# Performance work log

Hardware: AMD Instinct MI355X
Metric: run time of the kernel (lower is better)

## Reference

```python
import jax, jax.numpy as jnp
import numpy as np

B, D, LC, LQ = 16, 512, 2048, 512
NEG_INF = -1e30


def setup_inputs() -> dict:
    key = jax.random.key(0)
    k1, k2, k3 = jax.random.split(key, 3)
    C = jax.random.normal(k1, (B, D, LC), dtype=jnp.float32)
    Q = jax.random.normal(k2, (B, D, LQ), dtype=jnp.float32)
    cmask = jnp.ones((B, LC), dtype=bool)
    qmask = jnp.ones((B, LQ), dtype=bool)
    lim = np.sqrt(1.0 / D)
    w = jax.random.uniform(k3, (3 * D,), dtype=jnp.float32, minval=-lim, maxval=lim)
    return {"C": C, "Q": Q, "cmask": cmask, "qmask": qmask, "w": w}


def reference(C, Q, cmask, qmask, w):
    d = C.shape[1]
    Cb = jnp.swapaxes(C, 1, 2)  # (B, Lc, d)
    Qb = jnp.swapaxes(Q, 1, 2)  # (B, Lq, d)
    w1, w2, w3 = w[:d], w[d:2 * d], w[2 * d:]
    # Trilinear similarity, decomposed: S[b,i,j] = C_i.w1 + Q_j.w2 + (C_i*w3).Q_j
    S = (Cb @ w1)[:, :, None] + (Qb @ w2)[:, None, :] \
        + jnp.einsum('bid,bjd->bij', Cb * w3, Qb)  # (B, Lc, Lq)
    S1 = jax.nn.softmax(jnp.where(qmask[:, None, :], S, NEG_INF), axis=2)
    S2 = jax.nn.softmax(jnp.where(cmask[:, :, None], S, NEG_INF), axis=1)
    A = S1 @ Qb                                     # (B, Lc, d)
    Bt = (S1 @ jnp.swapaxes(S2, 1, 2)) @ Cb         # (B, Lc, d)
    out = jnp.concatenate([Cb, A, Cb * A, Cb * Bt], axis=2)  # (B, Lc, 4d)
    return jnp.swapaxes(out, 1, 2)  # (B, 4d, Lc); dropout inactive at inference
```

## Files before the change

kernel.cpp:

```cpp
#include <hip/hip_runtime.h>
#include <stdint.h>

#define Bn 16
#define Dn 512
#define LCn 2048
#define LQn 512

typedef __attribute__((ext_vector_type(8))) short s8v;
typedef __attribute__((ext_vector_type(4))) float f4v;

__device__ __forceinline__ unsigned short f2bf(float f) {
  union { float f; uint32_t u; } v; v.f = f;
  uint32_t r = v.u + 0x7FFFu + ((v.u >> 16) & 1u);
  return (unsigned short)(r >> 16);
}

__device__ __forceinline__ void async16(void* lds, const void* g) {
  __builtin_amdgcn_global_load_lds((const __attribute__((address_space(1))) void*)g,
                                   (__attribute__((address_space(3))) void*)lds, 16, 0, 0);
}

#define WAITVM(N) asm volatile("s_waitcnt vmcnt(" #N ")")
#define WAITLGKM(N) asm volatile("s_waitcnt lgkmcnt(" #N ")")
#define SCHEDBAR __builtin_amdgcn_sched_barrier(0)
#define BARRIER_LDS { WAITLGKM(0); SCHEDBAR; __builtin_amdgcn_s_barrier(); SCHEDBAR; }

typedef __attribute__((address_space(3))) const unsigned short* lds_csp;
__device__ __forceinline__ s8v ldsr(const unsigned short* p) {
  s8v r;
  asm volatile("ds_read_b128 %0, %1" : "=v"(r) : "v"((lds_csp)p));
  return r;
}



template <int KSTEPS>
__device__ __forceinline__ void gemm_core_p(const unsigned short* __restrict__ Ap,
                                            const unsigned short* __restrict__ Bp,
                                            unsigned short* As, unsigned short* Bs,
                                            f4v acc[4][4]) {
  const int t = threadIdx.x;
  const int lane = t & 63, quad = lane >> 4, l16 = lane & 15;
  const int wm = (t >> 6) & 1, wn = t >> 7;
  auto stage = [&](int buf, int ks) {
    const unsigned short* a = Ap + (size_t)ks * 4096;
    const unsigned short* b = Bp + (size_t)ks * 4096;
    async16(As + buf + t * 8, a + t * 8);
    async16(As + buf + (t + 256) * 8, a + 2048 + t * 8);
    async16(Bs + buf + t * 8, b + t * 8);
    async16(Bs + buf + (t + 256) * 8, b + 2048 + t * 8);
  };
  stage(0, 0);
  stage(4096, 1);
  for (int ks = 0; ks < KSTEPS; ++ks) {
    const int cur = (ks & 1) ? 4096 : 0;
    if (ks < KSTEPS - 1) { WAITVM(4); } else { WAITVM(0); }
    __builtin_amdgcn_s_barrier();
    SCHEDBAR;
    s8v af[4], bf[4];
#pragma unroll
    for (int mt = 0; mt < 4; ++mt)
      af[mt] = ldsr(As + cur + (wm * 64 + mt * 16 + l16) * 32 + quad * 8);
#pragma unroll
    for (int nt = 0; nt < 4; ++nt)
      bf[nt] = ldsr(Bs + cur + (wn * 64 + nt * 16 + l16) * 32 + quad * 8);
    WAITLGKM(0);
    SCHEDBAR;
    __builtin_amdgcn_s_barrier();
    SCHEDBAR;
    if (ks + 2 < KSTEPS) stage(cur, ks + 2);
    __builtin_amdgcn_s_setprio(1);
#pragma unroll
    for (int mt = 0; mt < 4; ++mt)
#pragma unroll
      for (int nt = 0; nt < 4; ++nt)
        acc[mt][nt] = __builtin_amdgcn_mfma_f32_16x16x32_bf16(af[mt], bf[nt], acc[mt][nt], 0, 0, 0);
    __builtin_amdgcn_s_setprio(0);
  }
}

template <int KSTEPS>
__device__ __forceinline__ void gemm_coreAB_p(const unsigned short* __restrict__ Ap,
                                              const unsigned short* __restrict__ Bp0,
                                              const unsigned short* __restrict__ Bp1,
                                              unsigned short* As, unsigned short* Bs0,
                                              unsigned short* Bs1,
                                              f4v accA[4][2], f4v accB[4][2]) {
  const int t = threadIdx.x;
  const int lane = t & 63, quad = lane >> 4, l16 = lane & 15;
  const int wm = (t >> 6) & 1, wn = t >> 7;
  auto stage = [&](int bufA, int bufB, int ks) {
    const unsigned short* a = Ap + (size_t)ks * 4096;
    async16(As + bufA + t * 8, a + t * 8);
    async16(As + bufA + (t + 256) * 8, a + 2048 + t * 8);
    async16(Bs0 + bufB + t * 8, Bp0 + (size_t)ks * 4096 + t * 8);
    async16(Bs1 + bufB + t * 8, Bp1 + (size_t)ks * 4096 + t * 8);
  };
  stage(0, 0, 0);
  stage(4096, 2048, 1);
  for (int ks = 0; ks < KSTEPS; ++ks) {
    const int curA = (ks & 1) ? 4096 : 0;
    const int curB = (ks & 1) ? 2048 : 0;
    if (ks < KSTEPS - 1) { WAITVM(4); } else { WAITVM(0); }
    __builtin_amdgcn_s_barrier();
    SCHEDBAR;
    s8v af[4], bq[2], bt[2];
#pragma unroll
    for (int mt = 0; mt < 4; ++mt)
      af[mt] = ldsr(As + curA + (wm * 64 + mt * 16 + l16) * 32 + quad * 8);
#pragma unroll
    for (int nt = 0; nt < 2; ++nt) {
      bq[nt] = ldsr(Bs0 + curB + (wn * 32 + nt * 16 + l16) * 32 + quad * 8);
      bt[nt] = ldsr(Bs1 + curB + (wn * 32 + nt * 16 + l16) * 32 + quad * 8);
    }
    WAITLGKM(0);
    SCHEDBAR;
    __builtin_amdgcn_s_barrier();
    SCHEDBAR;
    if (ks + 2 < KSTEPS) stage(curA, curB, ks + 2);
    __builtin_amdgcn_s_setprio(1);
#pragma unroll
    for (int mt = 0; mt < 4; ++mt)
#pragma unroll
      for (int nt = 0; nt < 2; ++nt) {
        accA[mt][nt] = __builtin_amdgcn_mfma_f32_16x16x32_bf16(af[mt], bq[nt], accA[mt][nt], 0, 0, 0);
        accB[mt][nt] = __builtin_amdgcn_mfma_f32_16x16x32_bf16(af[mt], bt[nt], accB[mt][nt], 0, 0, 0);
      }
    __builtin_amdgcn_s_setprio(0);
  }
}

template <int KSTEPS>
__device__ __forceinline__ void gemm_coreT_p(const unsigned short* __restrict__ Ap,
                                             const unsigned short* __restrict__ Bp,
                                             unsigned short* As, unsigned short* Bs,
                                             f4v acc[4][2]) {
  const int t = threadIdx.x;
  const int lane = t & 63, quad = lane >> 4, l16 = lane & 15;
  const int wm = (t >> 6) & 1, wn = t >> 7;
  auto stage = [&](int bufA, int bufB, int ks) {
    const unsigned short* a = Ap + (size_t)ks * 4096;
    async16(As + bufA + t * 8, a + t * 8);
    async16(As + bufA + (t + 256) * 8, a + 2048 + t * 8);
    async16(Bs + bufB + t * 8, Bp + (size_t)ks * 4096 + t * 8);
  };
  stage(0, 0, 0);
  stage(4096, 2048, 1);
  for (int ks = 0; ks < KSTEPS; ++ks) {
    const int curA = (ks & 1) ? 4096 : 0;
    const int curB = (ks & 1) ? 2048 : 0;
    if (ks < KSTEPS - 1) { WAITVM(3); } else { WAITVM(0); }
    __builtin_amdgcn_s_barrier();
    SCHEDBAR;
    s8v af[4], bf[2];
#pragma unroll
    for (int mt = 0; mt < 4; ++mt)
      af[mt] = ldsr(As + curA + (wm * 64 + mt * 16 + l16) * 32 + quad * 8);
#pragma unroll
    for (int nt = 0; nt < 2; ++nt)
      bf[nt] = ldsr(Bs + curB + (wn * 32 + nt * 16 + l16) * 32 + quad * 8);
    WAITLGKM(0);
    SCHEDBAR;
    __builtin_amdgcn_s_barrier();
    SCHEDBAR;
    if (ks + 2 < KSTEPS) stage(curA, curB, ks + 2);
    __builtin_amdgcn_s_setprio(1);
#pragma unroll
    for (int mt = 0; mt < 4; ++mt)
#pragma unroll
      for (int nt = 0; nt < 2; ++nt)
        acc[mt][nt] = __builtin_amdgcn_mfma_f32_16x16x32_bf16(af[mt], bf[nt], acc[mt][nt], 0, 0, 0);
    __builtin_amdgcn_s_setprio(0);
  }
}

#define EPILOGUE_IDS                                              \
  const int t = threadIdx.x, lane = t & 63, quad = lane >> 4,     \
            l16 = lane & 15;                                      \
  const int wave = t >> 6, wm = wave & 1, wn = wave >> 1;         \
  (void)lane; (void)wave;


__global__ __launch_bounds__(256) void k_castC(const float* __restrict__ C,
                                               const float* __restrict__ w,
                                               unsigned short* __restrict__ CbfP,
                                               unsigned short* __restrict__ CtP,
                                               float* __restrict__ cw) {
  __shared__ unsigned short tile[64][264];
  __shared__ float red[4][256];
  const int b = blockIdx.z, i0 = blockIdx.x * 256, d0 = blockIdx.y * 64;
  const int t = threadIdx.x;
  const int rq = t >> 6;
  const int i4 = (t & 63) * 4;
  f4v part = {0.f, 0.f, 0.f, 0.f};
#pragma unroll
  for (int p = 0; p < 16; ++p) {
    const int dl = p * 4 + rq;
    const f4v v = *(const f4v*)(C + ((size_t)b * Dn + d0 + dl) * LCn + i0 + i4);
    const float wd = w[d0 + dl];
#pragma unroll
    for (int r = 0; r < 4; ++r) {
      tile[dl][i4 + r] = f2bf(v[r]);
      part[r] += v[r] * wd;
    }
  }
  *(f4v*)(&red[rq][i4]) = part;
  __syncthreads();
  if (t < 64) {
    const int i = t * 4;
    f4v s = *(const f4v*)(&red[0][i]);
    s += *(const f4v*)(&red[1][i]);
    s += *(const f4v*)(&red[2][i]);
    s += *(const f4v*)(&red[3][i]);
#pragma unroll
    for (int r = 0; r < 4; ++r) atomicAdd(&cw[b * LCn + i0 + i + r], s[r]);
  }
  const size_t cbfT = (size_t)(b * 4 + (d0 >> 7)) * 64 + (i0 >> 5);
  const int row = t >> 2, k8 = (t & 3) * 8;
#pragma unroll
  for (int c = 0; c < 8; ++c)
    *(s8v*)(CbfP + (cbfT + c) * 4096 + ((d0 & 64) + row) * 32 + k8) =
        *(const s8v*)(&tile[row][c * 32 + k8]);
  const size_t ctT = (size_t)(b * 16 + (i0 >> 7)) * 16 + (d0 >> 5);
#pragma unroll
  for (int ti = 0; ti < 2; ++ti)
#pragma unroll
    for (int c = 0; c < 2; ++c)
#pragma unroll
      for (int q = 0; q < 2; ++q) {
        const int irow = q * 64 + (t >> 2);
        s8v v;
#pragma unroll
        for (int u = 0; u < 8; ++u)
          ((unsigned short*)&v)[u] = tile[c * 32 + k8 + u][ti * 128 + irow];
        *(s8v*)(CtP + (ctT + ti * 16 + c) * 4096 + irow * 32 + k8) = v;
      }
}

__global__ __launch_bounds__(256) void k_castQ(const float* __restrict__ Q,
                                               const float* __restrict__ w,
                                               unsigned short* __restrict__ QbfP,
                                               unsigned short* __restrict__ Q3tP,
                                               float* __restrict__ qw) {
  __shared__ unsigned short tile[64][66];
  __shared__ float red[4][64];
  const int b = blockIdx.z, j0 = blockIdx.x * 64, d0 = blockIdx.y * 64;
  const int t = threadIdx.x, jl = t & 63, dq = t >> 6;
  const size_t qbfT = (size_t)(b * 4 + (d0 >> 7)) * 16 + (j0 >> 5);
  float part = 0.f;
#pragma unroll 4
  for (int r = 0; r < 16; ++r) {
    const int dl = r * 4 + dq;
    const float v = Q[((size_t)b * Dn + d0 + dl) * LQn + j0 + jl];
    QbfP[(qbfT + (jl >> 5)) * 4096 + ((d0 & 64) + dl) * 32 + (jl & 31)] = f2bf(v);
    tile[dl][jl] = f2bf(v * w[2 * Dn + d0 + dl]);
    part += v * w[Dn + d0 + dl];
  }
  red[dq][jl] = part;
  __syncthreads();
  if (t < 64) {
    atomicAdd(&qw[b * LQn + j0 + t], red[0][t] + red[1][t] + red[2][t] + red[3][t]);
  }
  const size_t q3T = (size_t)(b * 4 + (j0 >> 7)) * 16 + (d0 >> 5);
  const int row = t >> 2, k8 = (t & 3) * 8;
#pragma unroll
  for (int c = 0; c < 2; ++c) {
    s8v v;
#pragma unroll
    for (int u = 0; u < 8; ++u)
      ((unsigned short*)&v)[u] = tile[c * 32 + k8 + u][row];
    *(s8v*)(Q3tP + (q3T + c) * 4096 + ((j0 & 64) + row) * 32 + k8) = v;
  }
}


union SmU {
  struct { unsigned short A[8192]; unsigned short B[8192]; } st;
  unsigned short e[4][64 * 72];
};

__global__ __launch_bounds__(256) void k_gemm1(
    const unsigned short* __restrict__ CtP, const unsigned short* __restrict__ Q3tP,
    const float* __restrict__ cw, const float* __restrict__ qw,
    unsigned short* __restrict__ EP, unsigned short* __restrict__ ETP,
    float* __restrict__ srow, float* __restrict__ scol) {
  __shared__ __align__(16) SmU sm;
  const int b = blockIdx.z, m0 = blockIdx.x * 128, n0 = blockIdx.y * 128;
  const unsigned short* Ap = CtP + ((size_t)(b * 16 + (m0 >> 7)) * 16) * 4096;
  const unsigned short* Bp = Q3tP + ((size_t)(b * 4 + (n0 >> 7)) * 16) * 4096;
  f4v acc[4][4];
#pragma unroll
  for (int i = 0; i < 4; ++i)
#pragma unroll
    for (int j = 0; j < 4; ++j) acc[i][j] = (f4v){0.f, 0.f, 0.f, 0.f};
  gemm_core_p<16>(Ap, Bp, sm.st.A, sm.st.B, acc);

  EPILOGUE_IDS
  const int R0 = m0 + wm * 64, C0 = n0 + wn * 64;
  float qws[4];
#pragma unroll
  for (int nt = 0; nt < 4; ++nt) qws[nt] = qw[b * LQn + C0 + nt * 16 + l16];
#pragma unroll
  for (int mt = 0; mt < 4; ++mt) {
    const f4v cw4 = *(const f4v*)(cw + b * LCn + R0 + mt * 16 + quad * 4);
#pragma unroll
    for (int nt = 0; nt < 4; ++nt)
#pragma unroll
      for (int r = 0; r < 4; ++r)
        acc[mt][nt][r] = __expf(acc[mt][nt][r] + cw4[r] + qws[nt]);
  }
#pragma unroll
  for (int mt = 0; mt < 4; ++mt)
#pragma unroll
    for (int r = 0; r < 4; ++r) {
      float v = acc[mt][0][r] + acc[mt][1][r] + acc[mt][2][r] + acc[mt][3][r];
      v += __shfl_xor(v, 1, 64);
      v += __shfl_xor(v, 2, 64);
      v += __shfl_xor(v, 4, 64);
      v += __shfl_xor(v, 8, 64);
      if (l16 == 0) atomicAdd(&srow[b * LCn + R0 + mt * 16 + quad * 4 + r], v);
    }
#pragma unroll
  for (int nt = 0; nt < 4; ++nt) {
    float v = 0.f;
#pragma unroll
    for (int mt = 0; mt < 4; ++mt)
#pragma unroll
      for (int r = 0; r < 4; ++r) v += acc[mt][nt][r];
    v += __shfl_xor(v, 16, 64);
    v += __shfl_xor(v, 32, 64);
    if (quad == 0) atomicAdd(&scol[b * LQn + C0 + nt * 16 + l16], v);
  }
  __syncthreads();
#pragma unroll
  for (int mt = 0; mt < 4; ++mt)
#pragma unroll
    for (int nt = 0; nt < 4; ++nt)
#pragma unroll
      for (int r = 0; r < 4; ++r)
        sm.e[wave][(mt * 16 + quad * 4 + r) * 72 + nt * 16 + l16] = f2bf(acc[mt][nt][r]);
  __syncthreads();
  {
    const size_t eT = (size_t)(b * 16 + (m0 >> 7)) * 16 + (n0 >> 5);
    const int row = t >> 1, half = t & 1;
#pragma unroll
    for (int c = 0; c < 4; ++c) {
      const unsigned short* src =
          sm.e[(row >> 6) | ((c >> 1) << 1)] + (row & 63) * 72 + (c & 1) * 32 + half * 16;
      unsigned short* dst = EP + (eT + c) * 4096 + row * 32 + half * 16;
      *(s8v*)(dst) = *(const s8v*)(src);
      *(s8v*)(dst + 8) = *(const s8v*)(src + 8);
    }
  }
  {
    const size_t etT = (size_t)(b * 4 + (n0 >> 7)) * 64 + (m0 >> 5);
    const int jrow = t >> 1, half = t & 1;
    const int jl = jrow & 63;
#pragma unroll
    for (int c = 0; c < 4; ++c) {
      const unsigned short* esrc = sm.e[(c >> 1) | ((jrow >> 6) << 1)];
      unsigned short* dst = ETP + (etT + c) * 4096 + jrow * 32 + half * 16;
#pragma unroll
      for (int u8 = 0; u8 < 2; ++u8) {
        const int ib = (c & 1) * 32 + half * 16 + u8 * 8;
        s8v v;
#pragma unroll
        for (int u = 0; u < 8; ++u)
          ((unsigned short*)&v)[u] = esrc[(ib + u) * 72 + jl];
        *(s8v*)(dst + u8 * 8) = v;
      }
    }
  }
}

__global__ __launch_bounds__(256) void k_gemmT(
    const unsigned short* __restrict__ ETP, const unsigned short* __restrict__ CbfP,
    const float* __restrict__ scol, unsigned short* __restrict__ TstP) {
  __shared__ __align__(16) union {
    struct { unsigned short A[8192]; unsigned short B[4096]; } st;
    unsigned short tt[64][136];
  } sm;
  const int b = blockIdx.z;
  const int m0 = blockIdx.x * 128;
  const int n0 = blockIdx.y * 64;
  const unsigned short* Ap = ETP + ((size_t)(b * 4 + (m0 >> 7)) * 64) * 4096;
  const unsigned short* Bp = CbfP + ((size_t)(b * 4 + (n0 >> 7)) * 64) * 4096 + (n0 & 64) * 32;
  f4v acc[4][2];
#pragma unroll
  for (int i = 0; i < 4; ++i)
#pragma unroll
    for (int j = 0; j < 2; ++j) acc[i][j] = (f4v){0.f, 0.f, 0.f, 0.f};
  gemm_coreT_p<64>(Ap, Bp, sm.st.A, sm.st.B, acc);

  EPILOGUE_IDS
  __syncthreads();
#pragma unroll
  for (int mt = 0; mt < 4; ++mt) {
    const int jl = wm * 64 + mt * 16 + quad * 4;
    const f4v sc = *(const f4v*)(scol + b * LQn + m0 + jl);
    f4v inv;
#pragma unroll
    for (int r = 0; r < 4; ++r) inv[r] = 1.0f / sc[r];
#pragma unroll
    for (int nt = 0; nt < 2; ++nt) {
      const int dl = wn * 32 + nt * 16 + l16;
#pragma unroll
      for (int r = 0; r < 4; ++r)
        sm.tt[dl][jl + r] = f2bf(acc[mt][nt][r] * inv[r]);
    }
  }
  __syncthreads();
  {
    const size_t tT = (size_t)(b * 4 + (n0 >> 7)) * 16 + (m0 >> 5);
    const int row = t >> 2, k8 = (t & 3) * 8;
#pragma unroll
    for (int c = 0; c < 4; ++c)
      *(s8v*)(TstP + (tT + c) * 4096 + ((n0 & 64) + row) * 32 + k8) =
          *(const s8v*)(&sm.tt[row][c * 32 + k8]);
  }
}

__global__ __launch_bounds__(256, 3) void k_gemmAB(
    const unsigned short* __restrict__ EP, const unsigned short* __restrict__ QbfP,
    const unsigned short* __restrict__ TstP, const float* __restrict__ srow,
    const float* __restrict__ C, float* __restrict__ out) {
  __shared__ __align__(16) union {
    struct { unsigned short A[8192]; unsigned short B0[4096]; unsigned short B1[4096]; } st;
    float ot[64][132];
  } sm;
  const int b = blockIdx.z, m0 = blockIdx.x * 128, n0 = blockIdx.y * 64;
  const unsigned short* Ap = EP + ((size_t)(b * 16 + (m0 >> 7)) * 16) * 4096;
  const unsigned short* Bp0 = QbfP + ((size_t)(b * 4 + (n0 >> 7)) * 16) * 4096 + (n0 & 64) * 32;
  const unsigned short* Bp1 = TstP + ((size_t)(b * 4 + (n0 >> 7)) * 16) * 4096 + (n0 & 64) * 32;
  f4v accA[4][2], accB[4][2];
#pragma unroll
  for (int i = 0; i < 4; ++i)
#pragma unroll
    for (int j = 0; j < 2; ++j) {
      accA[i][j] = (f4v){0.f, 0.f, 0.f, 0.f};
      accB[i][j] = (f4v){0.f, 0.f, 0.f, 0.f};
    }
  gemm_coreAB_p<16>(Ap, Bp0, Bp1, sm.st.A, sm.st.B0, sm.st.B1, accA, accB);

  EPILOGUE_IDS
  const int Ri = m0 + wm * 64;
  f4v inv[4];
#pragma unroll
  for (int mt = 0; mt < 4; ++mt) {
    const f4v sr4 = *(const f4v*)(srow + b * LCn + Ri + mt * 16 + quad * 4);
#pragma unroll
    for (int r = 0; r < 4; ++r) inv[mt][r] = 1.0f / sr4[r];
  }
  const int orow = t >> 5, ocol = (t & 31) * 4;
  const float* Cg = C + ((size_t)b * Dn + n0) * LCn + m0;
  float* outb = out + (size_t)b * (4 * Dn) * LCn;
  {
    float* o0 = outb + (size_t)n0 * LCn + m0;
#pragma unroll
    for (int p = 0; p < 8; ++p) {
      const int row = p * 8 + orow;
      const f4v v = *(const f4v*)(Cg + (size_t)row * LCn + ocol);
      *(f4v*)(&sm.ot[row][ocol]) = v;
      *(f4v*)(o0 + (size_t)row * LCn + ocol) = v;
    }
  }
  BARRIER_LDS
  f4v cfr[4][2];
#pragma unroll
  for (int mt = 0; mt < 4; ++mt)
#pragma unroll
    for (int nt = 0; nt < 2; ++nt)
      cfr[mt][nt] = *(const f4v*)(&sm.ot[wn * 32 + nt * 16 + l16][wm * 64 + mt * 16 + quad * 4]);
  BARRIER_LDS
#pragma unroll
  for (int s = 1; s <= 3; ++s) {
#pragma unroll
    for (int mt = 0; mt < 4; ++mt)
#pragma unroll
      for (int nt = 0; nt < 2; ++nt) {
        f4v v;
#pragma unroll
        for (int r = 0; r < 4; ++r) {
          const float a4 = accA[mt][nt][r] * inv[mt][r];
          const float b4 = accB[mt][nt][r] * inv[mt][r];
          v[r] = (s == 1) ? a4 : (s == 2) ? cfr[mt][nt][r] * a4 : cfr[mt][nt][r] * b4;
        }
        *(f4v*)(&sm.ot[wn * 32 + nt * 16 + l16][wm * 64 + mt * 16 + quad * 4]) = v;
      }
    BARRIER_LDS
    float* os = outb + ((size_t)s * Dn + n0) * LCn + m0;
#pragma unroll
    for (int p = 0; p < 8; ++p) {
      const int row = p * 8 + orow;
      *(f4v*)(os + (size_t)row * LCn + ocol) = *(const f4v*)(&sm.ot[row][ocol]);
    }
    if (s < 3) BARRIER_LDS
  }
}

extern "C" void kernel_launch(void* const* d_in, const int* in_sizes, int n_in,
                              void* d_out, int out_size, void* d_ws, size_t ws_size,
                              hipStream_t stream) {
  (void)in_sizes; (void)n_in; (void)out_size; (void)ws_size;
  const float* C = (const float*)d_in[0];
  const float* Q = (const float*)d_in[1];
  const float* w = (const float*)d_in[4];
  float* out = (float*)d_out;

  char* ws = (char*)d_ws;
  size_t off = 0;
  auto alloc = [&](size_t bytes) {
    char* p = ws + off;
    off += (bytes + 255) & ~(size_t)255;
    return p;
  };
  unsigned short* CbfP = (unsigned short*)alloc((size_t)Bn * Dn * LCn * 2);
  unsigned short* CtP  = (unsigned short*)alloc((size_t)Bn * LCn * Dn * 2);
  unsigned short* QbfP = (unsigned short*)alloc((size_t)Bn * Dn * LQn * 2);
  unsigned short* Q3tP = (unsigned short*)alloc((size_t)Bn * LQn * Dn * 2);
  unsigned short* EP   = (unsigned short*)alloc((size_t)Bn * LCn * LQn * 2);
  unsigned short* ETP  = (unsigned short*)alloc((size_t)Bn * LQn * LCn * 2);
  unsigned short* TstP = (unsigned short*)alloc((size_t)Bn * Dn * LQn * 2);
  float* stats = (float*)alloc((size_t)(2 * Bn * LCn + 2 * Bn * LQn) * 4);
  float* cw = stats;
  float* qw = cw + Bn * LCn;
  float* srow = qw + Bn * LQn;
  float* scol = srow + Bn * LCn;

  hipMemsetAsync(stats, 0, (size_t)(2 * Bn * LCn + 2 * Bn * LQn) * 4, stream);
  k_castC<<<dim3(LCn / 256, Dn / 64, Bn), 256, 0, stream>>>(C, w, CbfP, CtP, cw);
  k_castQ<<<dim3(LQn / 64, Dn / 64, Bn), 256, 0, stream>>>(Q, w, QbfP, Q3tP, qw);
  k_gemm1<<<dim3(LCn / 128, LQn / 128, Bn), 256, 0, stream>>>(CtP, Q3tP, cw, qw, EP, ETP, srow, scol);
  k_gemmT<<<dim3(LQn / 128, Dn / 64, Bn), 256, 0, stream>>>(ETP, CbfP, scol, TstP);
  k_gemmAB<<<dim3(LCn / 128, Dn / 64, Bn), 256, 0, stream>>>(EP, QbfP, TstP, srow, C, out);
}
```

Baseline: 468.2 us.

## Merge C and Q cast kernels into one launch and vectorize Q cast

The separate castC and castQ kernels are combined into a single k_cast launch, with blocks 0-7 handling C tiles and blocks 8-11 handling Q tiles through a shared-memory union. The Q path is rewritten to load float4 vectors over 128-wide column tiles and stage both the bf16 Q and the w3-scaled copy in LDS, so the packed QbfP layout is written with 16-byte stores instead of scalar ones. k_gemm1 also gains a launch-bounds occupancy hint of 4 blocks per SM. The intent is to remove one launch and its tail, and to make the Q cast memory traffic coalesced. The cost is a larger shared-memory footprint for the Q blocks, and the occupancy hint may raise register pressure in gemm1.

```diff
diff --git a/kernel.cpp b/kernel.cpp
--- a/kernel.cpp
+++ b/kernel.cpp
@@ -181,14 +181,17 @@
   (void)lane; (void)wave;
 
 
-__global__ __launch_bounds__(256) void k_castC(const float* __restrict__ C,
-                                               const float* __restrict__ w,
-                                               unsigned short* __restrict__ CbfP,
-                                               unsigned short* __restrict__ CtP,
-                                               float* __restrict__ cw) {
-  __shared__ unsigned short tile[64][264];
-  __shared__ float red[4][256];
-  const int b = blockIdx.z, i0 = blockIdx.x * 256, d0 = blockIdx.y * 64;
+union CastSm {
+  struct { unsigned short tile[64][264]; float red[4][256]; } c;
+  struct { unsigned short tq[64][136]; unsigned short tw[64][136];
+           float red[8][128]; } q;
+};
+
+__device__ __forceinline__ void castC_body(
+    CastSm& sm, int bx, const float* __restrict__ C, const float* __restrict__ w,
+    unsigned short* __restrict__ CbfP, unsigned short* __restrict__ CtP,
+    float* __restrict__ cw) {
+  const int b = blockIdx.z, i0 = bx * 256, d0 = blockIdx.y * 64;
   const int t = threadIdx.x;
   const int rq = t >> 6;
   const int i4 = (t & 63) * 4;
@@ -200,18 +203,18 @@
     const float wd = w[d0 + dl];
 #pragma unroll
     for (int r = 0; r < 4; ++r) {
-      tile[dl][i4 + r] = f2bf(v[r]);
+      sm.c.tile[dl][i4 + r] = f2bf(v[r]);
       part[r] += v[r] * wd;
     }
   }
-  *(f4v*)(&red[rq][i4]) = part;
+  *(f4v*)(&sm.c.red[rq][i4]) = part;
   __syncthreads();
   if (t < 64) {
     const int i = t * 4;
-    f4v s = *(const f4v*)(&red[0][i]);
-    s += *(const f4v*)(&red[1][i]);
-    s += *(const f4v*)(&red[2][i]);
-    s += *(const f4v*)(&red[3][i]);
+    f4v s = *(const f4v*)(&sm.c.red[0][i]);
+    s += *(const f4v*)(&sm.c.red[1][i]);
+    s += *(const f4v*)(&sm.c.red[2][i]);
+    s += *(const f4v*)(&sm.c.red[3][i]);
 #pragma unroll
     for (int r = 0; r < 4; ++r) atomicAdd(&cw[b * LCn + i0 + i + r], s[r]);
   }
@@ -220,7 +223,7 @@
 #pragma unroll
   for (int c = 0; c < 8; ++c)
     *(s8v*)(CbfP + (cbfT + c) * 4096 + ((d0 & 64) + row) * 32 + k8) =
-        *(const s8v*)(&tile[row][c * 32 + k8]);
+        *(const s8v*)(&sm.c.tile[row][c * 32 + k8]);
   const size_t ctT = (size_t)(b * 16 + (i0 >> 7)) * 16 + (d0 >> 5);
 #pragma unroll
   for (int ti = 0; ti < 2; ++ti)
@@ -232,45 +235,73 @@
         s8v v;
 #pragma unroll
         for (int u = 0; u < 8; ++u)
-          ((unsigned short*)&v)[u] = tile[c * 32 + k8 + u][ti * 128 + irow];
+          ((unsigned short*)&v)[u] = sm.c.tile[c * 32 + k8 + u][ti * 128 + irow];
         *(s8v*)(CtP + (ctT + ti * 16 + c) * 4096 + irow * 32 + k8) = v;
       }
 }
 
-__global__ __launch_bounds__(256) void k_castQ(const float* __restrict__ Q,
-                                               const float* __restrict__ w,
-                                               unsigned short* __restrict__ QbfP,
-                                               unsigned short* __restrict__ Q3tP,
-                                               float* __restrict__ qw) {
-  __shared__ unsigned short tile[64][66];
-  __shared__ float red[4][64];
-  const int b = blockIdx.z, j0 = blockIdx.x * 64, d0 = blockIdx.y * 64;
-  const int t = threadIdx.x, jl = t & 63, dq = t >> 6;
+__device__ __forceinline__ void castQ_body(
+    CastSm& sm, int bxq, const float* __restrict__ Q, const float* __restrict__ w,
+    unsigned short* __restrict__ QbfP, unsigned short* __restrict__ Q3tP,
+    float* __restrict__ qw) {
+  const int b = blockIdx.z, j0 = bxq * 128, d0 = blockIdx.y * 64;
+  const int t = threadIdx.x;
+  const int dq = t >> 5;
+  const int j4 = (t & 31) * 4;
+  f4v part = {0.f, 0.f, 0.f, 0.f};
+#pragma unroll
+  for (int p = 0; p < 8; ++p) {
+    const int dl = p * 8 + dq;
+    const f4v v = *(const f4v*)(Q + ((size_t)b * Dn + d0 + dl) * LQn + j0 + j4);
+    const float w2 = w[Dn + d0 + dl];
+    const float w3 = w[2 * Dn + d0 + dl];
+#pragma unroll
+    for (int r = 0; r < 4; ++r) {
+      sm.q.tq[dl][j4 + r] = f2bf(v[r]);
+      sm.q.tw[dl][j4 + r] = f2bf(v[r] * w3);
+      part[r] += v[r] * w2;
+    }
+  }
+  *(f4v*)(&sm.q.red[dq][j4]) = part;
+  __syncthreads();
+  if (t < 32) {
+    const int j = t * 4;
+    f4v s = *(const f4v*)(&sm.q.red[0][j]);
+#pragma unroll
+    for (int k = 1; k < 8; ++k) s += *(const f4v*)(&sm.q.red[k][j]);
+#pragma unroll
+    for (int r = 0; r < 4; ++r) atomicAdd(&qw[b * LQn + j0 + j + r], s[r]);
+  }
   const size_t qbfT = (size_t)(b * 4 + (d0 >> 7)) * 16 + (j0 >> 5);
-  float part = 0.f;
-#pragma unroll 4
-  for (int r = 0; r < 16; ++r) {
-    const int dl = r * 4 + dq;
-    const float v = Q[((size_t)b * Dn + d0 + dl) * LQn + j0 + jl];
-    QbfP[(qbfT + (jl >> 5)) * 4096 + ((d0 & 64) + dl) * 32 + (jl & 31)] = f2bf(v);
-    tile[dl][jl] = f2bf(v * w[2 * Dn + d0 + dl]);
-    part += v * w[Dn + d0 + dl];
-  }
-  red[dq][jl] = part;
-  __syncthreads();
-  if (t < 64) {
-    atomicAdd(&qw[b * LQn + j0 + t], red[0][t] + red[1][t] + red[2][t] + red[3][t]);
-  }
+  const int row = t >> 2, k8 = (t & 3) * 8;
+#pragma unroll
+  for (int c = 0; c < 4; ++c)
+    *(s8v*)(QbfP + (qbfT + c) * 4096 + ((d0 & 64) + row) * 32 + k8) =
+        *(const s8v*)(&sm.q.tq[row][c * 32 + k8]);
   const size_t q3T = (size_t)(b * 4 + (j0 >> 7)) * 16 + (d0 >> 5);
-  const int row = t >> 2, k8 = (t & 3) * 8;
-#pragma unroll
-  for (int c = 0; c < 2; ++c) {
-    s8v v;
-#pragma unroll
-    for (int u = 0; u < 8; ++u)
-      ((unsigned short*)&v)[u] = tile[c * 32 + k8 + u][row];
-    *(s8v*)(Q3tP + (q3T + c) * 4096 + ((j0 & 64) + row) * 32 + k8) = v;
-  }
+#pragma unroll
+  for (int c = 0; c < 2; ++c)
+#pragma unroll
+    for (int qq = 0; qq < 2; ++qq) {
+      const int jrow = qq * 64 + (t >> 2);
+      s8v v;
+#pragma unroll
+      for (int u = 0; u < 8; ++u)
+        ((unsigned short*)&v)[u] = sm.q.tw[c * 32 + k8 + u][jrow];
+      *(s8v*)(Q3tP + (q3T + c) * 4096 + jrow * 32 + k8) = v;
+    }
+}
+
+__global__ __launch_bounds__(256) void k_cast(
+    const float* __restrict__ C, const float* __restrict__ Q,
+    const float* __restrict__ w,
+    unsigned short* __restrict__ CbfP, unsigned short* __restrict__ CtP,
+    unsigned short* __restrict__ QbfP, unsigned short* __restrict__ Q3tP,
+    float* __restrict__ cw, float* __restrict__ qw) {
+  __shared__ __align__(16) CastSm sm;
+  const int bx = blockIdx.x;
+  if (bx < 8) castC_body(sm, bx, C, w, CbfP, CtP, cw);
+  else        castQ_body(sm, bx - 8, Q, w, QbfP, Q3tP, qw);
 }
 
 
@@ -279,7 +310,7 @@
   unsigned short e[4][64 * 72];
 };
 
-__global__ __launch_bounds__(256) void k_gemm1(
+__global__ __launch_bounds__(256, 4) void k_gemm1(
     const unsigned short* __restrict__ CtP, const unsigned short* __restrict__ Q3tP,
     const float* __restrict__ cw, const float* __restrict__ qw,
     unsigned short* __restrict__ EP, unsigned short* __restrict__ ETP,
@@ -528,8 +559,7 @@
   float* scol = srow + Bn * LCn;
 
   hipMemsetAsync(stats, 0, (size_t)(2 * Bn * LCn + 2 * Bn * LQn) * 4, stream);
-  k_castC<<<dim3(LCn / 256, Dn / 64, Bn), 256, 0, stream>>>(C, w, CbfP, CtP, cw);
-  k_castQ<<<dim3(LQn / 64, Dn / 64, Bn), 256, 0, stream>>>(Q, w, QbfP, Q3tP, qw);
+  k_cast<<<dim3(12, Dn / 64, Bn), 256, 0, stream>>>(C, Q, w, CbfP, CtP, QbfP, Q3tP, cw, qw);
   k_gemm1<<<dim3(LCn / 128, LQn / 128, Bn), 256, 0, stream>>>(CtP, Q3tP, cw, qw, EP, ETP, srow, scol);
   k_gemmT<<<dim3(LQn / 128, Dn / 64, Bn), 256, 0, stream>>>(ETP, CbfP, scol, TstP);
   k_gemmAB<<<dim3(LCn / 128, Dn / 64, Bn), 256, 0, stream>>>(EP, QbfP, TstP, srow, C, out);
```

Result: faster. 448.5 us (-4.2%).
